# Kernel optimization log

Hardware: AMD Instinct MI355X
Metric: run time of the kernel (lower is better)

Reference implementation:

```python
import jax, jax.numpy as jnp
import numpy as np

D = 512        # feat_dim
H_ENC = 8      # motion_encoder heads
H_SA = 4       # semantic-aware attention heads
BS, L, N = 8, 512, 4096
LN_EPS = 1e-5


def _layernorm(x, g, b):
    m = jnp.mean(x, axis=-1, keepdims=True)
    v = jnp.var(x, axis=-1, keepdims=True)
    return (x - m) * jax.lax.rsqrt(v + LN_EPS) * g + b


def _linear(x, w, b):
    # torch nn.Linear convention: w [out, in]
    return x @ w.T + b


def setup_inputs() -> dict:
    key = jax.random.key(0)
    ks = jax.random.split(key, 24)
    s = 0.02
    inp = {
        "motion": jax.random.normal(ks[0], (BS, L, D), jnp.float32),
        "scene_xyz": jax.random.normal(ks[1], (BS, N, 3), jnp.float32),
        "scene_feats": jax.random.normal(ks[2], (BS, N, D), jnp.float32),
        "spatial_prior": jax.random.normal(ks[3], (BS, L, N), jnp.float32),
        # motion_encoder (pre-norm MHA + pre-norm MLP, both residual)
        "enc_ln1_g": jnp.ones((D,), jnp.float32),
        "enc_ln1_b": jnp.zeros((D,), jnp.float32),
        "enc_qkv_w": jax.random.normal(ks[4], (3 * D, D), jnp.float32) * s,
        "enc_qkv_b": jnp.zeros((3 * D,), jnp.float32),
        "enc_out_w": jax.random.normal(ks[5], (D, D), jnp.float32) * s,
        "enc_out_b": jnp.zeros((D,), jnp.float32),
        "enc_ln2_g": jnp.ones((D,), jnp.float32),
        "enc_ln2_b": jnp.zeros((D,), jnp.float32),
        "enc_ff1_w": jax.random.normal(ks[6], (D, D), jnp.float32) * s,
        "enc_ff1_b": jnp.zeros((D,), jnp.float32),
        "enc_ff2_w": jax.random.normal(ks[7], (D, D), jnp.float32) * s,
        "enc_ff2_b": jnp.zeros((D,), jnp.float32),
        # SemanticAwareAttention
        "sa_q_w": jax.random.normal(ks[8], (D, D), jnp.float32) * s,
        "sa_q_b": jnp.zeros((D,), jnp.float32),
        "sa_kv_w": jax.random.normal(ks[9], (2 * D, D), jnp.float32) * s,
        "sa_kv_b": jnp.zeros((2 * D,), jnp.float32),
        "sa_out_w": jax.random.normal(ks[10], (D, D), jnp.float32) * s,
        "sa_out_b": jnp.zeros((D,), jnp.float32),
        # final concat-MLP: in 2D -> 4D -> D  (Mlp(2D, D, expansion=4))
        "mlp_fc1_w": jax.random.normal(ks[11], (4 * D, 2 * D), jnp.float32) * s,
        "mlp_fc1_b": jnp.zeros((4 * D,), jnp.float32),
        "mlp_fc2_w": jax.random.normal(ks[12], (D, 4 * D), jnp.float32) * s,
        "mlp_fc2_b": jnp.zeros((D,), jnp.float32),
    }
    return inp


def _forward(motion, scene_xyz, scene_feats, spatial_prior,
             enc_ln1_g, enc_ln1_b, enc_qkv_w, enc_qkv_b, enc_out_w, enc_out_b,
             enc_ln2_g, enc_ln2_b, enc_ff1_w, enc_ff1_b, enc_ff2_w, enc_ff2_b,
             sa_q_w, sa_q_b, sa_kv_w, sa_kv_b, sa_out_w, sa_out_b,
             mlp_fc1_w, mlp_fc1_b, mlp_fc2_w, mlp_fc2_b):
    bs, slen, _ = motion.shape
    n = scene_feats.shape[1]
    dh_enc = D // H_ENC
    dh_sa = D // H_SA

    # ---- motion encoder: pre-norm MHA + residual ----
    h = _layernorm(motion, enc_ln1_g, enc_ln1_b)
    qkv = _linear(h, enc_qkv_w, enc_qkv_b)                      # [bs, L, 3D]
    q, k, v = jnp.split(qkv, 3, axis=-1)
    q = q.reshape(bs, slen, H_ENC, dh_enc)
    k = k.reshape(bs, slen, H_ENC, dh_enc)
    v = v.reshape(bs, slen, H_ENC, dh_enc)
    att = jnp.einsum("bqhd,bkhd->bhqk", q, k) * (dh_enc ** -0.5)
    att = jax.nn.softmax(att, axis=-1)
    o = jnp.einsum("bhqk,bkhd->bqhd", att, v).reshape(bs, slen, D)
    x = motion + _linear(o, enc_out_w, enc_out_b)

    # ---- pre-norm MLP + residual ----
    h2 = _layernorm(x, enc_ln2_g, enc_ln2_b)
    ff = _linear(jax.nn.gelu(_linear(h2, enc_ff1_w, enc_ff1_b), approximate=False),
                 enc_ff2_w, enc_ff2_b)
    motion_sca = x + ff

    # ---- SemanticAwareAttention ----
    q = _linear(motion_sca, sa_q_w, sa_q_b) * (D ** -0.5)       # scale by feat_dim (faithful)
    kv = _linear(scene_feats, sa_kv_w, sa_kv_b)
    k, v = jnp.split(kv, 2, axis=-1)
    # faithful to torch: q.view(bs, H, L, d) splits heads from flattened (L, D)
    q = q.reshape(bs, H_SA, slen, dh_sa)
    k = k.reshape(bs, n, H_SA, dh_sa).transpose(0, 2, 1, 3)     # [bs, H, N, d]
    v = v.reshape(bs, n, H_SA, dh_sa).transpose(0, 2, 1, 3)
    att = jnp.einsum("bhqd,bhkd->bhqk", q, k) + spatial_prior[:, None, :, :]
    att = jax.nn.softmax(att, axis=-1)
    sm = jnp.einsum("bhqk,bhkd->bqhd", att, v).reshape(bs, slen, D)
    sm_feature = _linear(sm, sa_out_w, sa_out_b)

    # ---- concat + MLP ----
    cat = jnp.concatenate([motion_sca, sm_feature], axis=-1)    # [bs, L, 2D]
    out = _linear(jax.nn.gelu(_linear(cat, mlp_fc1_w, mlp_fc1_b), approximate=False),
                  mlp_fc2_w, mlp_fc2_b)
    return out


def reference(motion, scene_xyz, scene_feats, spatial_prior,
              enc_ln1_g, enc_ln1_b, enc_qkv_w, enc_qkv_b, enc_out_w, enc_out_b,
              enc_ln2_g, enc_ln2_b, enc_ff1_w, enc_ff1_b, enc_ff2_w, enc_ff2_b,
              sa_q_w, sa_q_b, sa_kv_w, sa_kv_b, sa_out_w, sa_out_b,
              mlp_fc1_w, mlp_fc1_b, mlp_fc2_w, mlp_fc2_b):
    return _forward(motion, scene_xyz, scene_feats, spatial_prior,
                    enc_ln1_g, enc_ln1_b, enc_qkv_w, enc_qkv_b, enc_out_w, enc_out_b,
                    enc_ln2_g, enc_ln2_b, enc_ff1_w, enc_ff1_b, enc_ff2_w, enc_ff2_b,
                    sa_q_w, sa_q_b, sa_kv_w, sa_kv_b, sa_out_w, sa_out_b,
                    mlp_fc1_w, mlp_fc1_b, mlp_fc2_w, mlp_fc2_b)
```

## Files before the change

kernel.cpp:

```cpp
#include <hip/hip_runtime.h>

typedef unsigned short bf16_t;
typedef __attribute__((ext_vector_type(8))) short bf16x8;
typedef __attribute__((ext_vector_type(4))) float f32x4;

__device__ __forceinline__ float bf2f(bf16_t u) {
  union { unsigned int i; float f; } v; v.i = ((unsigned int)u) << 16; return v.f;
}
__device__ __forceinline__ bf16_t f2bf(float f) {
  union { float f; unsigned int i; } v; v.f = f;
  unsigned int u = v.i;
  u += 0x7fffu + ((u >> 16) & 1u);
  return (bf16_t)(u >> 16);
}
__device__ __forceinline__ float gelu_exact(float x) {
  return 0.5f * x * (1.0f + erff(x * 0.7071067811865475f));
}
__device__ __forceinline__ void g2l16(bf16_t* l, const bf16_t* g) {
  __builtin_amdgcn_global_load_lds(
      (const __attribute__((address_space(1))) unsigned int*)g,
      (__attribute__((address_space(3))) unsigned int*)l, 16, 0, 0);
}

__global__ __launch_bounds__(256) void f2bf_kernel(const float4* __restrict__ s,
                                                   ushort4* __restrict__ d, int n4) {
  int i = blockIdx.x * 256 + threadIdx.x;
  if (i < n4) {
    float4 f = s[i];
    ushort4 u; u.x = f2bf(f.x); u.y = f2bf(f.y); u.z = f2bf(f.z); u.w = f2bf(f.w);
    d[i] = u;
  }
}

__global__ __launch_bounds__(256) void ln_kernel(const float* __restrict__ x,
                                                 const float* __restrict__ g,
                                                 const float* __restrict__ bta,
                                                 bf16_t* __restrict__ y) {
  const int w = threadIdx.x >> 6, lane = threadIdx.x & 63;
  const long row = (long)blockIdx.x * 4 + w;
  const long base = row * 512;
  const int c0 = lane << 2;
  float v[8];
  float4 f0 = *(const float4*)(x + base + c0);
  float4 f1 = *(const float4*)(x + base + 256 + c0);
  v[0]=f0.x; v[1]=f0.y; v[2]=f0.z; v[3]=f0.w;
  v[4]=f1.x; v[5]=f1.y; v[6]=f1.z; v[7]=f1.w;
  float s = 0.f;
#pragma unroll
  for (int c=0;c<8;++c) s += v[c];
#pragma unroll
  for (int o=32;o>0;o>>=1) s += __shfl_xor(s, o);
  const float mean = s * 0.001953125f;
  float ss = 0.f;
#pragma unroll
  for (int c=0;c<8;++c) { float d = v[c]-mean; ss += d*d; }
#pragma unroll
  for (int o=32;o>0;o>>=1) ss += __shfl_xor(ss, o);
  const float rstd = rsqrtf(ss * 0.001953125f + 1e-5f);
  ushort4 o0, o1;
  o0.x = f2bf((v[0]-mean)*rstd*g[c0+0] + bta[c0+0]);
  o0.y = f2bf((v[1]-mean)*rstd*g[c0+1] + bta[c0+1]);
  o0.z = f2bf((v[2]-mean)*rstd*g[c0+2] + bta[c0+2]);
  o0.w = f2bf((v[3]-mean)*rstd*g[c0+3] + bta[c0+3]);
  o1.x = f2bf((v[4]-mean)*rstd*g[256+c0+0] + bta[256+c0+0]);
  o1.y = f2bf((v[5]-mean)*rstd*g[256+c0+1] + bta[256+c0+1]);
  o1.z = f2bf((v[6]-mean)*rstd*g[256+c0+2] + bta[256+c0+2]);
  o1.w = f2bf((v[7]-mean)*rstd*g[256+c0+3] + bta[256+c0+3]);
  *(ushort4*)(y + base + c0) = o0;
  *(ushort4*)(y + base + 256 + c0) = o1;
}

struct MmaNT {
  const bf16_t* A; const bf16_t* W; const float* bias; const float* res; void* C;
  long lda, sAb, sAh;
  long ldw, sWb, sWh;
  long ldr, sRb, sRh;
  long ldc, sCb, sCh;
  int K, zdiv, cBf, act;
  float scale;
};

template <int MT>
__global__ __launch_bounds__(256) void mma_nt_kernel(MmaNT p) {
  constexpr int FM = MT / 32;
  constexpr int TILE_E = (MT + 128) * 32;
  constexpr int ST_E = MT * 128;
  constexpr int SM_E = (TILE_E > ST_E) ? TILE_E : ST_E;
  __shared__ __align__(16) bf16_t smem[SM_E];
  bf16_t* Al = smem;
  bf16_t* Wl = smem + MT * 32;
  const int tid = threadIdx.x;
  const int wid = tid >> 6, lane = tid & 63;
  const int wm = wid & 1, wn = wid >> 1;
  const int quad = lane >> 4, l16 = lane & 15;
  const int z = blockIdx.z;
  const int zb = z / p.zdiv, zh = z % p.zdiv;

  const int nbx = gridDim.x;
  const int nwg = nbx * gridDim.y;
  const int flat = blockIdx.y * nbx + blockIdx.x;
  const int sw = (flat & 7) * (nwg >> 3) + (flat >> 3);
  const int bx = sw % nbx, by = sw / nbx;

  const long m0 = (long)by * MT;
  const long n0 = (long)bx * 128;

  f32x4 zero4 = {0.f, 0.f, 0.f, 0.f};
  f32x4 acc[FM][4];
#pragma unroll
  for (int fm = 0; fm < FM; ++fm)
#pragma unroll
    for (int fn = 0; fn < 4; ++fn) acc[fm][fn] = zero4;

  if constexpr (MT == 128) {
    const bf16_t* Ag = p.A + (long)zb * p.sAb + (long)zh * p.sAh + m0 * p.lda;
    const bf16_t* Wg = p.W + (long)zb * p.sWb + (long)zh * p.sWh + n0 * p.ldw;
    const int sr = lane >> 2;
    const int sc = (lane & 3) * 8;
    for (int kc = 0; kc < p.K; kc += 32) {
#pragma unroll
      for (int j = 0; j < 2; ++j)
        g2l16(&Al[(j * 64 + wid * 16) * 32],
              Ag + (long)(j * 64 + wid * 16 + sr) * p.lda + kc + sc);
#pragma unroll
      for (int j = 0; j < 2; ++j)
        g2l16(&Wl[(j * 64 + wid * 16) * 32],
              Wg + (long)(j * 64 + wid * 16 + sr) * p.ldw + kc + sc);
      __syncthreads();
      bf16x8 af[FM], wf[4];
#pragma unroll
      for (int fm = 0; fm < FM; ++fm)
        af[fm] = *(const bf16x8*)&Al[(wm * 64 + fm * 16 + l16) * 32 + quad * 8];
#pragma unroll
      for (int fn = 0; fn < 4; ++fn)
        wf[fn] = *(const bf16x8*)&Wl[(wn * 64 + fn * 16 + l16) * 32 + quad * 8];
#pragma unroll
      for (int fm = 0; fm < FM; ++fm)
#pragma unroll
        for (int fn = 0; fn < 4; ++fn)
          acc[fm][fn] = __builtin_amdgcn_mfma_f32_16x16x32_bf16(af[fm], wf[fn], acc[fm][fn], 0, 0, 0);
      __syncthreads();
    }
  } else {
    const bf16_t* Ag = p.A + (long)zb * p.sAb + (long)zh * p.sAh +
                       (m0 + wm * (MT / 2) + l16) * p.lda;
    const bf16_t* Wg = p.W + (long)zb * p.sWb + (long)zh * p.sWh +
                       (n0 + wn * 64 + l16) * p.ldw;
    bf16x8 af[FM], wf[4];
#pragma unroll
    for (int fm = 0; fm < FM; ++fm)
      af[fm] = *(const bf16x8*)(Ag + (long)(fm * 16) * p.lda + quad * 8);
#pragma unroll
    for (int fn = 0; fn < 4; ++fn)
      wf[fn] = *(const bf16x8*)(Wg + (long)(fn * 16) * p.ldw + quad * 8);
    for (int kc = 0; kc < p.K; kc += 32) {
      bf16x8 afn[FM], wfn[4];
      const int kn = kc + 32;
      if (kn < p.K) {
#pragma unroll
        for (int fm = 0; fm < FM; ++fm)
          afn[fm] = *(const bf16x8*)(Ag + (long)(fm * 16) * p.lda + kn + quad * 8);
#pragma unroll
        for (int fn = 0; fn < 4; ++fn)
          wfn[fn] = *(const bf16x8*)(Wg + (long)(fn * 16) * p.ldw + kn + quad * 8);
      }
#pragma unroll
      for (int fm = 0; fm < FM; ++fm)
#pragma unroll
        for (int fn = 0; fn < 4; ++fn)
          acc[fm][fn] = __builtin_amdgcn_mfma_f32_16x16x32_bf16(af[fm], wf[fn], acc[fm][fn], 0, 0, 0);
#pragma unroll
      for (int fm = 0; fm < FM; ++fm) af[fm] = afn[fm];
#pragma unroll
      for (int fn = 0; fn < 4; ++fn) wf[fn] = wfn[fn];
    }
  }

  const long cOff = (long)zb * p.sCb + (long)zh * p.sCh;
  const long rOff = (long)zb * p.sRb + (long)zh * p.sRh;
  if (p.cBf) {
#pragma unroll
    for (int fm = 0; fm < FM; ++fm) {
#pragma unroll
      for (int fn = 0; fn < 4; ++fn) {
        const int lc = wn * 64 + fn * 16 + l16;
        const long col = n0 + lc;
        const float bv = p.bias ? p.bias[col] : 0.f;
#pragma unroll
        for (int r = 0; r < 4; ++r) {
          const int lr = wm * (MT / 2) + fm * 16 + quad * 4 + r;
          float t = acc[fm][fn][r] + bv;
          if (p.act) t = gelu_exact(t);
          t *= p.scale;
          if (p.res) t += p.res[rOff + (m0 + lr) * p.ldr + col];
          smem[lr * 128 + lc] = f2bf(t);
        }
      }
    }
    __syncthreads();
    bf16_t* Cg = (bf16_t*)p.C + cOff + m0 * p.ldc + n0;
#pragma unroll
    for (int i = 0; i < MT / 16; ++i) {
      const int flat2 = tid + i * 256;
      const int r = flat2 >> 4, c = (flat2 & 15) * 8;
      *(uint4*)(Cg + (long)r * p.ldc + c) = *(const uint4*)&smem[r * 128 + c];
    }
  } else {
#pragma unroll
    for (int fm = 0; fm < FM; ++fm) {
#pragma unroll
      for (int fn = 0; fn < 4; ++fn) {
        const long col = n0 + wn * 64 + fn * 16 + l16;
        const float bv = p.bias ? p.bias[col] : 0.f;
#pragma unroll
        for (int r = 0; r < 4; ++r) {
          const long row = m0 + wm * (MT / 2) + fm * 16 + quad * 4 + r;
          float t = acc[fm][fn][r] + bv;
          if (p.act) t = gelu_exact(t);
          t *= p.scale;
          if (p.res) t += p.res[rOff + row * p.ldr + col];
          ((float*)p.C)[cOff + row * p.ldc + col] = t;
        }
      }
    }
  }
}

struct TransP {
  const bf16_t* src; bf16_t* dst;
  long sSb, sSh, ld;
  int nh, N, D;
};

__global__ __launch_bounds__(256) void transpose_kernel(TransP p) {
  __shared__ bf16_t T[64][72];
  const int tid = threadIdx.x;
  const int z = blockIdx.z;
  const int zb = z / p.nh, zh = z % p.nh;
  const long n0 = (long)blockIdx.x * 64;
  const long d0 = (long)blockIdx.y * 64;
  const bf16_t* src = p.src + (long)zb * p.sSb + (long)zh * p.sSh;
  bf16_t* dst = p.dst + (long)z * p.D * p.N;
#pragma unroll
  for (int i = 0; i < 2; ++i) {
    int flat = tid + i * 256, r = flat >> 3, cg = flat & 7;
    uint4 v = *(const uint4*)(src + (n0 + r) * p.ld + d0 + cg * 8);
    *(uint4*)&T[r][cg * 8] = v;
  }
  __syncthreads();
#pragma unroll
  for (int i = 0; i < 2; ++i) {
    int flat = tid + i * 256, dr = flat >> 3, ncg = flat & 7;
    uint4 o;
    unsigned int* op = (unsigned int*)&o;
#pragma unroll
    for (int j = 0; j < 4; ++j)
      op[j] = (unsigned int)T[ncg * 8 + 2 * j][dr] | ((unsigned int)T[ncg * 8 + 2 * j + 1][dr] << 16);
    *(uint4*)(dst + (d0 + dr) * p.N + n0 + ncg * 8) = o;
  }
}

struct FlashP2 {
  const bf16_t* Q; const bf16_t* K; const bf16_t* VT; const float* prior;
  float* partO; float* partML;
  long ldq, sQb, sQh;
  long ldk, sKb, sKh;
  long sVz, sPb;
  int nh, N, segN;
  float scale;
};

template <int DH, int HASP>
__global__ __launch_bounds__(256) void flash3_kernel(FlashP2 p) {
  constexpr int KK = DH / 32;
  constexpr int NFO = DH / 16;
  constexpr int KE = 64 * DH;
  constexpr int VE = DH * 64;
  constexpr int PE = 64 * 72;
  constexpr int SM_E = (DH == 128) ? (KE + VE) : (KE + VE + PE);
  __shared__ __align__(16) bf16_t smem[SM_E];
  bf16_t* Kl = smem;
  bf16_t* Vl = smem + KE;
  bf16_t* Pl = (DH == 128) ? smem : (smem + KE + VE);
  const int tid = threadIdx.x;
  const int w = tid >> 6, lane = tid & 63;
  const int quad = lane >> 4, l16 = lane & 15;
  const int z = blockIdx.z;
  const int zb = z / p.nh, zh = z % p.nh;
  const int qr0 = blockIdx.y * 64 + w * 16;
  const bf16_t* Q = p.Q + (long)zb * p.sQb + (long)zh * p.sQh + (long)qr0 * p.ldq;
  const bf16_t* K = p.K + (long)zb * p.sKb + (long)zh * p.sKh;
  const bf16_t* VT = p.VT + (long)z * p.sVz;

  bf16x8 qf[KK];
#pragma unroll
  for (int kk = 0; kk < KK; ++kk)
    qf[kk] = *(const bf16x8*)(Q + (long)l16 * p.ldq + kk * 32 + quad * 8);

  f32x4 zero4 = {0.f, 0.f, 0.f, 0.f};
  f32x4 O[NFO];
  float m_[4], l_[4];
#pragma unroll
  for (int f = 0; f < NFO; ++f) O[f] = zero4;
#pragma unroll
  for (int r = 0; r < 4; ++r) { m_[r] = -1e30f; l_[r] = 0.f; }

  constexpr int LPR = DH / 8;
  constexpr int RPC = 512 / DH;
  const int krl = lane / LPR;
  const int kcb = (lane % LPR) * 16;
  const int vrl = lane >> 3;
  const int vcb = (lane & 7) * 16;

  const int k0 = blockIdx.x * p.segN;
  for (int kt = k0; kt < k0 + p.segN; kt += 64) {
    __syncthreads();
#pragma unroll
    for (int j = 0; j < DH / 32; ++j) {
      const int R0 = (w + 4 * j) * RPC;
      const int r = R0 + krl;
      const int cs = kcb ^ ((r & 7) << 4);
      g2l16(&Kl[R0 * DH], K + (long)(kt + r) * p.ldk + (cs >> 1));
    }
#pragma unroll
    for (int j = 0; j < DH / 32; ++j) {
      const int R0 = (w + 4 * j) * 8;
      const int r = R0 + vrl;
      const int cs = vcb ^ ((r & 7) << 4);
      g2l16(&Vl[R0 * 64], VT + (long)r * p.N + kt + (cs >> 1));
    }
    float pr[4][4];
    if (HASP) {
      const float* PR = p.prior + (long)zb * p.sPb +
                        (long)(qr0 + quad * 4) * p.N + kt;
#pragma unroll
      for (int nf = 0; nf < 4; ++nf)
#pragma unroll
        for (int r = 0; r < 4; ++r)
          pr[nf][r] = PR[(long)r * p.N + nf * 16 + l16];
    }
    __syncthreads();
    f32x4 s[4];
#pragma unroll
    for (int nf = 0; nf < 4; ++nf) s[nf] = zero4;
#pragma unroll
    for (int nf = 0; nf < 4; ++nf)
#pragma unroll
      for (int kk = 0; kk < KK; ++kk) {
        bf16x8 kf = *(const bf16x8*)&Kl[(nf * 16 + l16) * DH +
                                        ((kk * 32 + quad * 8) ^ ((l16 & 7) << 3))];
        s[nf] = __builtin_amdgcn_mfma_f32_16x16x32_bf16(qf[kk], kf, s[nf], 0, 0, 0);
      }
    float tm[4];
#pragma unroll
    for (int r = 0; r < 4; ++r) tm[r] = -1e30f;
#pragma unroll
    for (int nf = 0; nf < 4; ++nf)
#pragma unroll
      for (int r = 0; r < 4; ++r) {
        float t = s[nf][r] * p.scale;
        if (HASP) t += pr[nf][r];
        s[nf][r] = t;
        tm[r] = fmaxf(tm[r], t);
      }
#pragma unroll
    for (int off = 1; off < 16; off <<= 1)
#pragma unroll
      for (int r = 0; r < 4; ++r) tm[r] = fmaxf(tm[r], __shfl_xor(tm[r], off));
    float alpha[4], rs[4];
#pragma unroll
    for (int r = 0; r < 4; ++r) {
      float mn = fmaxf(m_[r], tm[r]);
      alpha[r] = __expf(m_[r] - mn);
      m_[r] = mn;
      rs[r] = 0.f;
    }
#pragma unroll
    for (int nf = 0; nf < 4; ++nf)
#pragma unroll
      for (int r = 0; r < 4; ++r) {
        float pv = __expf(s[nf][r] - m_[r]);
        s[nf][r] = pv;
        rs[r] += pv;
      }
#pragma unroll
    for (int off = 1; off < 16; off <<= 1)
#pragma unroll
      for (int r = 0; r < 4; ++r) rs[r] += __shfl_xor(rs[r], off);
#pragma unroll
    for (int r = 0; r < 4; ++r) l_[r] = l_[r] * alpha[r] + rs[r];
    if (DH == 128) __syncthreads();
#pragma unroll
    for (int nf = 0; nf < 4; ++nf)
#pragma unroll
      for (int r = 0; r < 4; ++r)
        Pl[(w * 16 + quad * 4 + r) * 72 + nf * 16 + l16] = f2bf(s[nf][r]);
#pragma unroll
    for (int f = 0; f < NFO; ++f)
#pragma unroll
      for (int r = 0; r < 4; ++r) O[f][r] *= alpha[r];
    bf16x8 pf[2];
#pragma unroll
    for (int kk2 = 0; kk2 < 2; ++kk2)
      pf[kk2] = *(const bf16x8*)&Pl[(w * 16 + l16) * 72 + kk2 * 32 + quad * 8];
#pragma unroll
    for (int f = 0; f < NFO; ++f)
#pragma unroll
      for (int kk2 = 0; kk2 < 2; ++kk2) {
        bf16x8 vf = *(const bf16x8*)&Vl[(f * 16 + l16) * 64 +
                                        ((kk2 * 32 + quad * 8) ^ ((l16 & 7) << 3))];
        O[f] = __builtin_amdgcn_mfma_f32_16x16x32_bf16(pf[kk2], vf, O[f], 0, 0, 0);
      }
  }
  const long t = ((long)z * gridDim.y + blockIdx.y) * gridDim.x + blockIdx.x;
  float* PO = p.partO + t * (64 * DH);
  float* PM = p.partML + t * 128;
  const int row = w * 16 + quad * 4;
#pragma unroll
  for (int f = 0; f < NFO; ++f)
#pragma unroll
    for (int r = 0; r < 4; ++r)
      PO[(long)(row + r) * DH + f * 16 + l16] = O[f][r];
  if (l16 == 0) {
#pragma unroll
    for (int r = 0; r < 4; ++r) {
      PM[(row + r) * 2 + 0] = m_[r];
      PM[(row + r) * 2 + 1] = l_[r];
    }
  }
}

struct MergeP {
  const float* partO; const float* partML; bf16_t* C;
  long ldc, sCb;
  int nh, y;
};

template <int DH, int NS>
__global__ __launch_bounds__(256) void fmerge_kernel(MergeP p) {
  const int tid = threadIdx.x;
  const int r = tid >> 2, ch = tid & 3;
  const int blk = blockIdx.x;
  const int z = blk / p.y, qb = blk % p.y;
  const int zb = z / p.nh, zh = z % p.nh;
  const long t0 = (long)blk * NS;
  float mm[NS], wgt[NS];
  float mstar = -1e30f;
#pragma unroll
  for (int s = 0; s < NS; ++s) {
    mm[s] = p.partML[(t0 + s) * 128 + r * 2];
    mstar = fmaxf(mstar, mm[s]);
  }
  float lsum = 0.f;
#pragma unroll
  for (int s = 0; s < NS; ++s) {
    wgt[s] = __expf(mm[s] - mstar);
    lsum += wgt[s] * p.partML[(t0 + s) * 128 + r * 2 + 1];
  }
  const float inv = 1.0f / lsum;
  const int c0 = ch * (DH / 4);
  bf16_t* Cp = p.C + (long)zb * p.sCb + (long)(qb * 64 + r) * p.ldc + (long)zh * DH + c0;
#pragma unroll
  for (int c = 0; c < DH / 4; c += 4) {
    float4 acc = make_float4(0.f, 0.f, 0.f, 0.f);
#pragma unroll
    for (int s = 0; s < NS; ++s) {
      float4 v = *(const float4*)(p.partO + (t0 + s) * (64 * DH) + (long)r * DH + c0 + c);
      acc.x += wgt[s] * v.x; acc.y += wgt[s] * v.y;
      acc.z += wgt[s] * v.z; acc.w += wgt[s] * v.w;
    }
    ushort4 o;
    o.x = f2bf(acc.x * inv); o.y = f2bf(acc.y * inv);
    o.z = f2bf(acc.z * inv); o.w = f2bf(acc.w * inv);
    *(ushort4*)(Cp + c) = o;
  }
}

#define MB(x) ((long)(x) << 20)

extern "C" void kernel_launch(void* const* d_in, const int* in_sizes, int n_in,
                              void* d_out, int out_size, void* d_ws, size_t ws_size,
                              hipStream_t stream) {
  const float* motion      = (const float*)d_in[0];
  const float* scene_feats = (const float*)d_in[2];
  const float* prior       = (const float*)d_in[3];
  const float* ln1_g = (const float*)d_in[4];
  const float* ln1_b = (const float*)d_in[5];
  const float* qkv_w = (const float*)d_in[6];
  const float* qkv_b = (const float*)d_in[7];
  const float* out_w = (const float*)d_in[8];
  const float* out_b = (const float*)d_in[9];
  const float* ln2_g = (const float*)d_in[10];
  const float* ln2_b = (const float*)d_in[11];
  const float* ff1_w = (const float*)d_in[12];
  const float* ff1_b = (const float*)d_in[13];
  const float* ff2_w = (const float*)d_in[14];
  const float* ff2_b = (const float*)d_in[15];
  const float* saq_w = (const float*)d_in[16];
  const float* saq_b = (const float*)d_in[17];
  const float* sakv_w = (const float*)d_in[18];
  const float* sakv_b = (const float*)d_in[19];
  const float* saout_w = (const float*)d_in[20];
  const float* saout_b = (const float*)d_in[21];
  const float* fc1_w = (const float*)d_in[22];
  const float* fc1_b = (const float*)d_in[23];
  const float* fc2_w = (const float*)d_in[24];
  const float* fc2_b = (const float*)d_in[25];

  char* W = (char*)d_ws;
  bf16_t* h_bf    = (bf16_t*)(W + MB(0));
  float*  x_f     = (float*) (W + MB(4));
  bf16_t* o_ff    = (bf16_t*)(W + MB(12));
  bf16_t* qkv_bf  = (bf16_t*)(W + MB(16));
  bf16_t* qsa     = (bf16_t*)(W + MB(28));
  bf16_t* sm_bf   = (bf16_t*)(W + MB(32));
  bf16_t* cat_bf  = (bf16_t*)(W + MB(36));
  bf16_t* fc1g    = (bf16_t*)(W + MB(44));
  bf16_t* vTe     = (bf16_t*)(W + MB(60));
  bf16_t* kv_bf   = (bf16_t*)(W + MB(64));
  bf16_t* vT      = (bf16_t*)(W + MB(128));
  bf16_t* wbase   = (bf16_t*)(W + MB(160));
  bf16_t* scene_bf= (bf16_t*)(W + MB(172));

  float* encO  = (float*)fc1g;
  float* encML = (float*)cat_bf;
  float* saO   = (float*)scene_bf;
  float* saML  = (float*)vTe;

  bf16_t* wq   = wbase + 0L;
  bf16_t* wout = wbase + 786432L;
  bf16_t* wff1 = wbase + 1048576L;
  bf16_t* wff2 = wbase + 1310720L;
  bf16_t* wsaq = wbase + 1572864L;
  bf16_t* wskv = wbase + 1835008L;
  bf16_t* wsout= wbase + 2359296L;
  bf16_t* wfc1 = wbase + 2621440L;
  bf16_t* wfc2 = wbase + 4718592L;

  const dim3 B256(256);
  auto cvt = [&](const float* s, bf16_t* d, long n) {
    int n4 = (int)(n / 4);
    f2bf_kernel<<<(n4 + 255) / 256, B256, 0, stream>>>((const float4*)s, (ushort4*)d, n4);
  };
  cvt(qkv_w,  wq,   786432);
  cvt(out_w,  wout, 262144);
  cvt(ff1_w,  wff1, 262144);
  cvt(ff2_w,  wff2, 262144);
  cvt(saq_w,  wsaq, 262144);
  cvt(sakv_w, wskv, 524288);
  cvt(saout_w,wsout,262144);
  cvt(fc1_w,  wfc1, 2097152);
  cvt(fc2_w,  wfc2, 1048576);
  cvt(scene_feats, scene_bf, 16777216);

  ln_kernel<<<1024, B256, 0, stream>>>(motion, ln1_g, ln1_b, h_bf);

  { MmaNT p{}; p.scale=1.f; p.zdiv=1; p.cBf=1;
    p.A=h_bf; p.lda=512; p.W=wq; p.ldw=512; p.bias=qkv_b;
    p.C=qkv_bf; p.ldc=1536; p.K=512;
    mma_nt_kernel<128><<<dim3(12,32,1), B256, 0, stream>>>(p); }

  { TransP t{}; t.src=qkv_bf+1024; t.dst=vTe; t.sSb=786432; t.sSh=64;
    t.ld=1536; t.nh=8; t.N=512; t.D=64;
    transpose_kernel<<<dim3(8,1,64), B256, 0, stream>>>(t); }
  { FlashP2 p{};
    p.Q=qkv_bf;     p.ldq=1536; p.sQb=786432; p.sQh=64;
    p.K=qkv_bf+512; p.ldk=1536; p.sKb=786432; p.sKh=64;
    p.VT=vTe; p.sVz=32768;
    p.prior=nullptr; p.sPb=0;
    p.partO=encO; p.partML=encML;
    p.nh=8; p.N=512; p.segN=256; p.scale=0.125f;
    flash3_kernel<64,0><<<dim3(2,8,64), B256, 0, stream>>>(p); }
  { MergeP m{}; m.partO=encO; m.partML=encML; m.C=o_ff;
    m.ldc=512; m.sCb=262144; m.nh=8; m.y=8;
    fmerge_kernel<64,2><<<512, B256, 0, stream>>>(m); }

  { MmaNT p{}; p.scale=1.f; p.zdiv=1;
    p.A=o_ff; p.lda=512; p.W=wout; p.ldw=512; p.bias=out_b;
    p.res=motion; p.ldr=512;
    p.C=x_f; p.ldc=512; p.K=512;
    mma_nt_kernel<64><<<dim3(4,64,1), B256, 0, stream>>>(p); }

  ln_kernel<<<1024, B256, 0, stream>>>(x_f, ln2_g, ln2_b, h_bf);

  { MmaNT p{}; p.scale=1.f; p.zdiv=1; p.cBf=1; p.act=1;
    p.A=h_bf; p.lda=512; p.W=wff1; p.ldw=512; p.bias=ff1_b;
    p.C=o_ff; p.ldc=512; p.K=512;
    mma_nt_kernel<64><<<dim3(4,64,1), B256, 0, stream>>>(p); }

  { MmaNT p{}; p.scale=1.f; p.zdiv=1; p.cBf=1;
    p.A=o_ff; p.lda=512; p.W=wff2; p.ldw=512; p.bias=ff2_b;
    p.res=x_f; p.ldr=512;
    p.C=cat_bf; p.ldc=1024; p.K=512;
    mma_nt_kernel<64><<<dim3(4,64,1), B256, 0, stream>>>(p); }

  { MmaNT p{}; p.zdiv=1; p.cBf=1; p.scale=0.04419417382415922f;
    p.A=cat_bf; p.lda=1024; p.W=wsaq; p.ldw=512; p.bias=saq_b;
    p.C=qsa; p.ldc=512; p.K=512;
    mma_nt_kernel<64><<<dim3(4,64,1), B256, 0, stream>>>(p); }

  { MmaNT p{}; p.scale=1.f; p.zdiv=1; p.cBf=1;
    p.A=scene_bf; p.lda=512; p.W=wskv; p.ldw=512; p.bias=sakv_b;
    p.C=kv_bf; p.ldc=1024; p.K=512;
    mma_nt_kernel<128><<<dim3(8,256,1), B256, 0, stream>>>(p); }

  { TransP t{}; t.src=kv_bf+512; t.dst=vT; t.sSb=4194304; t.sSh=128;
    t.ld=1024; t.nh=4; t.N=4096; t.D=128;
    transpose_kernel<<<dim3(64,2,32), B256, 0, stream>>>(t); }
  { FlashP2 p{};
    p.Q=qsa;   p.ldq=128;  p.sQb=262144;  p.sQh=65536;
    p.K=kv_bf; p.ldk=1024; p.sKb=4194304; p.sKh=128;
    p.VT=vT; p.sVz=524288;
    p.prior=prior; p.sPb=2097152;
    p.partO=saO; p.partML=saML;
    p.nh=4; p.N=4096; p.segN=1024; p.scale=1.f;
    flash3_kernel<128,1><<<dim3(4,8,32), B256, 0, stream>>>(p); }
  { MergeP m{}; m.partO=saO; m.partML=saML; m.C=sm_bf;
    m.ldc=512; m.sCb=262144; m.nh=4; m.y=8;
    fmerge_kernel<128,4><<<256, B256, 0, stream>>>(m); }

  { MmaNT p{}; p.scale=1.f; p.zdiv=1; p.cBf=1;
    p.A=sm_bf; p.lda=512; p.W=wsout; p.ldw=512; p.bias=saout_b;
    p.C=cat_bf + 512; p.ldc=1024; p.K=512;
    mma_nt_kernel<64><<<dim3(4,64,1), B256, 0, stream>>>(p); }

  { MmaNT p{}; p.scale=1.f; p.zdiv=1; p.cBf=1; p.act=1;
    p.A=cat_bf; p.lda=1024; p.W=wfc1; p.ldw=1024; p.bias=fc1_b;
    p.C=fc1g; p.ldc=2048; p.K=1024;
    mma_nt_kernel<128><<<dim3(16,32,1), B256, 0, stream>>>(p); }

  { MmaNT p{}; p.scale=1.f; p.zdiv=1;
    p.A=fc1g; p.lda=2048; p.W=wfc2; p.ldw=2048; p.bias=fc2_b;
    p.C=d_out; p.ldc=512; p.K=2048;
    mma_nt_kernel<64><<<dim3(4,64,1), B256, 0, stream>>>(p); }
}
```

Measured before the change: 684.4 us.

## Prefetch spatial prior one tile ahead and skip unneeded softmax rescales

The flash-attention loop now loads the spatial-prior tile for the next K/V block into registers during the current block, using a two-buffer ping-pong with the loop unrolled by two. This hides the global prior-load latency behind the QK MFMAs. It also adds a lazy online-softmax rescale: the running max and O/l are rescaled only when some row's tile max exceeds the stored max by more than 8. This skips the per-tile exp and O multiply in most iterations. Costs are extra registers, and an implicit requirement that segN be a multiple of 128. With the lazy rescale, exp values can reach up to e^8 before bf16 conversion.

Measured after the change: 670.5 us. 2.0% less time.

```diff
diff --git a/kernel.cpp b/kernel.cpp
--- a/kernel.cpp
+++ b/kernel.cpp
@@ -312,34 +312,47 @@
   const int vrl = lane >> 3;
   const int vcb = (lane & 7) * 16;
 
+  const float* PRrow = HASP ? (p.prior + (long)zb * p.sPb +
+                               (long)(qr0 + quad * 4) * p.N) : (const float*)nullptr;
+
   const int k0 = blockIdx.x * p.segN;
-  for (int kt = k0; kt < k0 + p.segN; kt += 64) {
+  const int kend = k0 + p.segN;
+
+  float pr0[4][4], pr1[4][4];
+  if (HASP) {
+#pragma unroll
+    for (int nf = 0; nf < 4; ++nf)
+#pragma unroll
+      for (int r = 0; r < 4; ++r)
+        pr0[nf][r] = PRrow[(long)r * p.N + k0 + nf * 16 + l16];
+  }
+
+  auto body = [&](int ktc, float (&prC)[4][4], float (&prN)[4][4]) {
     __syncthreads();
 #pragma unroll
     for (int j = 0; j < DH / 32; ++j) {
       const int R0 = (w + 4 * j) * RPC;
       const int r = R0 + krl;
       const int cs = kcb ^ ((r & 7) << 4);
-      g2l16(&Kl[R0 * DH], K + (long)(kt + r) * p.ldk + (cs >> 1));
+      g2l16(&Kl[R0 * DH], K + (long)(ktc + r) * p.ldk + (cs >> 1));
     }
 #pragma unroll
     for (int j = 0; j < DH / 32; ++j) {
       const int R0 = (w + 4 * j) * 8;
       const int r = R0 + vrl;
       const int cs = vcb ^ ((r & 7) << 4);
-      g2l16(&Vl[R0 * 64], VT + (long)r * p.N + kt + (cs >> 1));
-    }
-    float pr[4][4];
+      g2l16(&Vl[R0 * 64], VT + (long)r * p.N + ktc + (cs >> 1));
+    }
+    __syncthreads();
     if (HASP) {
-      const float* PR = p.prior + (long)zb * p.sPb +
-                        (long)(qr0 + quad * 4) * p.N + kt;
+      int kn = ktc + 64;
+      if (kn > p.N - 64) kn = p.N - 64;
 #pragma unroll
       for (int nf = 0; nf < 4; ++nf)
 #pragma unroll
         for (int r = 0; r < 4; ++r)
-          pr[nf][r] = PR[(long)r * p.N + nf * 16 + l16];
-    }
-    __syncthreads();
+          prN[nf][r] = PRrow[(long)r * p.N + kn + nf * 16 + l16];
+    }
     f32x4 s[4];
 #pragma unroll
     for (int nf = 0; nf < 4; ++nf) s[nf] = zero4;
@@ -359,7 +372,7 @@
 #pragma unroll
       for (int r = 0; r < 4; ++r) {
         float t = s[nf][r] * p.scale;
-        if (HASP) t += pr[nf][r];
+        if (HASP) t += prC[nf][r];
         s[nf][r] = t;
         tm[r] = fmaxf(tm[r], t);
       }
@@ -367,14 +380,25 @@
     for (int off = 1; off < 16; off <<= 1)
 #pragma unroll
       for (int r = 0; r < 4; ++r) tm[r] = fmaxf(tm[r], __shfl_xor(tm[r], off));
-    float alpha[4], rs[4];
-#pragma unroll
-    for (int r = 0; r < 4; ++r) {
-      float mn = fmaxf(m_[r], tm[r]);
-      alpha[r] = __expf(m_[r] - mn);
-      m_[r] = mn;
-      rs[r] = 0.f;
-    }
+    const int ok = (tm[0] <= m_[0] + 8.f) && (tm[1] <= m_[1] + 8.f) &&
+                   (tm[2] <= m_[2] + 8.f) && (tm[3] <= m_[3] + 8.f);
+    if (!__all(ok)) {
+      float alpha[4];
+#pragma unroll
+      for (int r = 0; r < 4; ++r) {
+        float mn = fmaxf(m_[r], tm[r]);
+        alpha[r] = __expf(m_[r] - mn);
+        m_[r] = mn;
+        l_[r] *= alpha[r];
+      }
+#pragma unroll
+      for (int f = 0; f < NFO; ++f)
+#pragma unroll
+        for (int r = 0; r < 4; ++r) O[f][r] *= alpha[r];
+    }
+    float rs[4];
+#pragma unroll
+    for (int r = 0; r < 4; ++r) rs[r] = 0.f;
 #pragma unroll
     for (int nf = 0; nf < 4; ++nf)
 #pragma unroll
@@ -388,17 +412,13 @@
 #pragma unroll
       for (int r = 0; r < 4; ++r) rs[r] += __shfl_xor(rs[r], off);
 #pragma unroll
-    for (int r = 0; r < 4; ++r) l_[r] = l_[r] * alpha[r] + rs[r];
+    for (int r = 0; r < 4; ++r) l_[r] += rs[r];
     if (DH == 128) __syncthreads();
 #pragma unroll
     for (int nf = 0; nf < 4; ++nf)
 #pragma unroll
       for (int r = 0; r < 4; ++r)
         Pl[(w * 16 + quad * 4 + r) * 72 + nf * 16 + l16] = f2bf(s[nf][r]);
-#pragma unroll
-    for (int f = 0; f < NFO; ++f)
-#pragma unroll
-      for (int r = 0; r < 4; ++r) O[f][r] *= alpha[r];
     bf16x8 pf[2];
 #pragma unroll
     for (int kk2 = 0; kk2 < 2; ++kk2)
@@ -411,7 +431,13 @@
                                         ((kk2 * 32 + quad * 8) ^ ((l16 & 7) << 3))];
         O[f] = __builtin_amdgcn_mfma_f32_16x16x32_bf16(pf[kk2], vf, O[f], 0, 0, 0);
       }
-  }
+  };
+
+  for (int kt = k0; kt < kend; kt += 128) {
+    body(kt, pr0, pr1);
+    body(kt + 64, pr1, pr0);
+  }
+
   const long t = ((long)z * gridDim.y + blockIdx.y) * gridDim.x + blockIdx.x;
   float* PO = p.partO + t * (64 * DH);
   float* PM = p.partML + t * 128;
```
